# Optimization experiments

Hardware: AMD Instinct MI355X
Metric: run time of the kernel (lower is better)

The kernel has to match this reference:

```python
import jax, jax.numpy as jnp
import numpy as np

B, C, H, W_ = 4, 3, 224, 224
K = 196          # max_segments
E = 768          # embed_dim


def setup_inputs() -> dict:
    key = jax.random.key(0)
    k1, k2, k3 = jax.random.split(key, 3)
    img = jax.random.normal(k1, (B, C, H, W_), dtype=jnp.float32)
    segments = jax.random.randint(k2, (B, H, W_), 0, K, dtype=jnp.int32)
    W = jax.random.normal(k3, (C, E), dtype=jnp.float32) * 0.02
    b = jnp.zeros((E,), dtype=jnp.float32)
    return {"img": img, "segments": segments, "W": W, "b": b}


def reference(img, segments, W, b):
    # Per-segment one-hot masked bucketing (the torch loop, vectorized):
    # segment_features[b,k,c,h,w] = img[b,c,h,w] * (segments[b,h,w] == k)
    onehot = jax.nn.one_hot(segments, K, dtype=img.dtype)           # (B,H,W,K)
    seg_feat = jnp.einsum('bhwk,bchw->bkchw', onehot, img)          # (B,K,C,H,W)
    # Feature extractor stand-in: spatial mean pool + linear C->E
    pooled = seg_feat.mean(axis=(3, 4))                              # (B,K,C)
    out = jnp.einsum('bkc,ce->bke', pooled, W) + b                   # (B,K,E)
    return out
```

## Files before the change

### kernel.cpp

```cpp
#include <hip/hip_runtime.h>

#define Bn  4
#define Cn  3
#define Hn  224
#define Wn  224
#define Kn  196
#define En  768
#define HW  (Hn * Wn)
#define BPB 49
#define PIX_PER_BLOCK (HW / BPB)
#define KC  (Kn * Cn)

__global__ __launch_bounds__(256) void seg_pool_kernel(
    const float* __restrict__ img,
    const int*   __restrict__ seg,
    float*       __restrict__ pooled)
{
    __shared__ float acc[KC];
    const int tid = threadIdx.x;
    for (int i = tid; i < KC; i += 256) acc[i] = 0.0f;
    __syncthreads();

    const int batch = blockIdx.x / BPB;
    const int blk   = blockIdx.x % BPB;
    const int p0    = blk * PIX_PER_BLOCK;

    const float* img0 = img + (size_t)batch * Cn * HW;
    const int*   seg0 = seg + (size_t)batch * HW;

    #pragma unroll
    for (int i = 0; i < PIX_PER_BLOCK; i += 256) {
        const int   p  = p0 + i + tid;
        const int   k  = seg0[p];
        const float v0 = img0[p];
        const float v1 = img0[HW + p];
        const float v2 = img0[2 * HW + p];
        atomicAdd(&acc[k * 3 + 0], v0);
        atomicAdd(&acc[k * 3 + 1], v1);
        atomicAdd(&acc[k * 3 + 2], v2);
    }
    __syncthreads();

    float* out0 = pooled + (size_t)batch * KC;
    for (int i = tid; i < KC; i += 256) atomicAdd(&out0[i], acc[i]);
}

__global__ __launch_bounds__(256) void embed_kernel(
    const float* __restrict__ pooled,
    const float* __restrict__ Wm,
    const float* __restrict__ bias,
    float*       __restrict__ out)
{
    const float inv = 1.0f / (float)HW;
    const int t  = blockIdx.x * 256 + threadIdx.x;
    const int e4 = t % (En / 4);
    const int bk = t / (En / 4);

    const float p0 = pooled[bk * 3 + 0] * inv;
    const float p1 = pooled[bk * 3 + 1] * inv;
    const float p2 = pooled[bk * 3 + 2] * inv;

    const float4 w0 = ((const float4*)(Wm          ))[e4];
    const float4 w1 = ((const float4*)(Wm +     En ))[e4];
    const float4 w2 = ((const float4*)(Wm + 2 * En ))[e4];
    const float4 bb = ((const float4*)bias)[e4];

    float4 r;
    r.x = p0 * w0.x + p1 * w1.x + p2 * w2.x + bb.x;
    r.y = p0 * w0.y + p1 * w1.y + p2 * w2.y + bb.y;
    r.z = p0 * w0.z + p1 * w1.z + p2 * w2.z + bb.z;
    r.w = p0 * w0.w + p1 * w1.w + p2 * w2.w + bb.w;
    ((float4*)out)[t] = r;
}

extern "C" void kernel_launch(void* const* d_in, const int* in_sizes, int n_in,
                              void* d_out, int out_size, void* d_ws, size_t ws_size,
                              hipStream_t stream) {
    const float* img  = (const float*)d_in[0];
    const int*   seg  = (const int*)  d_in[1];
    const float* Wm   = (const float*)d_in[2];
    const float* bias = (const float*)d_in[3];
    float* out    = (float*)d_out;
    float* pooled = (float*)d_ws;

    hipMemsetAsync(pooled, 0, (size_t)Bn * KC * sizeof(float), stream);

    seg_pool_kernel<<<Bn * BPB, 256, 0, stream>>>(img, seg, pooled);

    embed_kernel<<<(Bn * Kn * En / 4) / 256, 256, 0, stream>>>(pooled, Wm, bias, out);
}
```

Baseline: 68.31 us.

## Replace global atomics and memset with per-block partials reduced in embed kernel

The pooling kernel now writes each block's shared-memory histogram to its own workspace slot instead of doing global atomicAdds, so the hipMemsetAsync launch is no longer needed. The embed kernel runs one block per (batch, segment), sums the 49 partials into the 3 channel sums in shared memory, then applies the linear layer. Pixel loads are vectorized to int4 and float4, giving each thread 4 pixels. This removes global atomic contention and one launch, at the cost of extra partial reads and a serial 49-term sum per embed block.

```diff
diff --git a/kernel.cpp b/kernel.cpp
--- a/kernel.cpp
+++ b/kernel.cpp
@@ -8,13 +8,13 @@
 #define En  768
 #define HW  (Hn * Wn)
 #define BPB 49
-#define PIX_PER_BLOCK (HW / BPB)
+#define NPOOL (Bn * BPB)
 #define KC  (Kn * Cn)
 
-__global__ __launch_bounds__(256) void seg_pool_kernel(
+__global__ __launch_bounds__(256) void seg_pool_partial(
     const float* __restrict__ img,
     const int*   __restrict__ seg,
-    float*       __restrict__ pooled)
+    float*       __restrict__ partials)
 {
     __shared__ float acc[KC];
     const int tid = threadIdx.x;
@@ -23,54 +23,76 @@
 
     const int batch = blockIdx.x / BPB;
     const int blk   = blockIdx.x % BPB;
-    const int p0    = blk * PIX_PER_BLOCK;
+    const int p4    = blk * 256 + tid;
 
-    const float* img0 = img + (size_t)batch * Cn * HW;
-    const int*   seg0 = seg + (size_t)batch * HW;
+    const int4*   seg4 = (const int4*)(seg + (size_t)batch * HW);
+    const float4* im   = (const float4*)(img + (size_t)batch * Cn * HW);
 
-    #pragma unroll
-    for (int i = 0; i < PIX_PER_BLOCK; i += 256) {
-        const int   p  = p0 + i + tid;
-        const int   k  = seg0[p];
-        const float v0 = img0[p];
-        const float v1 = img0[HW + p];
-        const float v2 = img0[2 * HW + p];
-        atomicAdd(&acc[k * 3 + 0], v0);
-        atomicAdd(&acc[k * 3 + 1], v1);
-        atomicAdd(&acc[k * 3 + 2], v2);
-    }
+    const int4   s  = seg4[p4];
+    const float4 v0 = im[p4];
+    const float4 v1 = im[HW / 4 + p4];
+    const float4 v2 = im[2 * (HW / 4) + p4];
+
+    atomicAdd(&acc[s.x * 3 + 0], v0.x);
+    atomicAdd(&acc[s.x * 3 + 1], v1.x);
+    atomicAdd(&acc[s.x * 3 + 2], v2.x);
+    atomicAdd(&acc[s.y * 3 + 0], v0.y);
+    atomicAdd(&acc[s.y * 3 + 1], v1.y);
+    atomicAdd(&acc[s.y * 3 + 2], v2.y);
+    atomicAdd(&acc[s.z * 3 + 0], v0.z);
+    atomicAdd(&acc[s.z * 3 + 1], v1.z);
+    atomicAdd(&acc[s.z * 3 + 2], v2.z);
+    atomicAdd(&acc[s.w * 3 + 0], v0.w);
+    atomicAdd(&acc[s.w * 3 + 1], v1.w);
+    atomicAdd(&acc[s.w * 3 + 2], v2.w);
     __syncthreads();
 
-    float* out0 = pooled + (size_t)batch * KC;
-    for (int i = tid; i < KC; i += 256) atomicAdd(&out0[i], acc[i]);
+    float4* dst = (float4*)(partials + (size_t)blockIdx.x * KC);
+    if (tid < KC / 4) dst[tid] = ((const float4*)acc)[tid];
 }
 
-__global__ __launch_bounds__(256) void embed_kernel(
-    const float* __restrict__ pooled,
+__global__ __launch_bounds__(192) void embed_kernel(
+    const float* __restrict__ partials,
     const float* __restrict__ Wm,
     const float* __restrict__ bias,
     float*       __restrict__ out)
 {
-    const float inv = 1.0f / (float)HW;
-    const int t  = blockIdx.x * 256 + threadIdx.x;
-    const int e4 = t % (En / 4);
-    const int bk = t / (En / 4);
+    __shared__ float part[BPB * 3];
+    __shared__ float sums[3];
+    const int b   = blockIdx.x / Kn;
+    const int k   = blockIdx.x % Kn;
+    const int tid = threadIdx.x;
 
-    const float p0 = pooled[bk * 3 + 0] * inv;
-    const float p1 = pooled[bk * 3 + 1] * inv;
-    const float p2 = pooled[bk * 3 + 2] * inv;
+    if (tid < BPB * 3) {
+        const int j = tid / 3;
+        const int c = tid % 3;
+        part[tid] = partials[(size_t)(b * BPB + j) * KC + k * 3 + c];
+    }
+    __syncthreads();
 
-    const float4 w0 = ((const float4*)(Wm          ))[e4];
-    const float4 w1 = ((const float4*)(Wm +     En ))[e4];
-    const float4 w2 = ((const float4*)(Wm + 2 * En ))[e4];
-    const float4 bb = ((const float4*)bias)[e4];
+    if (tid < 3) {
+        float s = 0.0f;
+        #pragma unroll
+        for (int j = 0; j < BPB; ++j) s += part[j * 3 + tid];
+        sums[tid] = s * (1.0f / (float)HW);
+    }
+    __syncthreads();
+
+    const float p0 = sums[0];
+    const float p1 = sums[1];
+    const float p2 = sums[2];
+
+    const float4 w0 = ((const float4*)(Wm          ))[tid];
+    const float4 w1 = ((const float4*)(Wm +     En ))[tid];
+    const float4 w2 = ((const float4*)(Wm + 2 * En ))[tid];
+    const float4 bb = ((const float4*)bias)[tid];
 
     float4 r;
     r.x = p0 * w0.x + p1 * w1.x + p2 * w2.x + bb.x;
     r.y = p0 * w0.y + p1 * w1.y + p2 * w2.y + bb.y;
     r.z = p0 * w0.z + p1 * w1.z + p2 * w2.z + bb.z;
     r.w = p0 * w0.w + p1 * w1.w + p2 * w2.w + bb.w;
-    ((float4*)out)[t] = r;
+    ((float4*)out)[(size_t)blockIdx.x * (En / 4) + tid] = r;
 }
 
 extern "C" void kernel_launch(void* const* d_in, const int* in_sizes, int n_in,
@@ -80,12 +102,9 @@
     const int*   seg  = (const int*)  d_in[1];
     const float* Wm   = (const float*)d_in[2];
     const float* bias = (const float*)d_in[3];
-    float* out    = (float*)d_out;
-    float* pooled = (float*)d_ws;
+    float* out      = (float*)d_out;
+    float* partials = (float*)d_ws;
 
-    hipMemsetAsync(pooled, 0, (size_t)Bn * KC * sizeof(float), stream);
-
-    seg_pool_kernel<<<Bn * BPB, 256, 0, stream>>>(img, seg, pooled);
-
-    embed_kernel<<<(Bn * Kn * En / 4) / 256, 256, 0, stream>>>(pooled, Wm, bias, out);
+    seg_pool_partial<<<NPOOL, 256, 0, stream>>>(img, seg, partials);
+    embed_kernel<<<Bn * Kn, 192, 0, stream>>>(partials, Wm, bias, out);
 }
```

Measured after the change: 66.37 us. 2.8% less time.
